# Kernel optimization log

Measured on AMD Instinct MI355X. Metric: run time of the kernel, lower is better.

Reference implementation:

```python
import jax, jax.numpy as jnp
import numpy as np

NEG_INF = -1e9  # large negative for masking (avoid NaN rows under -inf with fully masked rows)
LEAKY_SLOPE = 0.2

def setup_inputs() -> dict:
    key = jax.random.key(0)
    k1, k2, k3, k4, k5 = jax.random.split(key, 5)
    N, in_dim, out_dim = 8192, 512, 64
    x = jax.random.normal(k1, (N, in_dim), dtype=jnp.float32)
    adj = jax.random.randint(k2, (N, N), 0, 2, dtype=jnp.int32)
    W = jax.random.normal(k3, (out_dim, in_dim), dtype=jnp.float32) * (1.0 / np.sqrt(in_dim))
    a_src = jax.random.normal(k4, (out_dim,), dtype=jnp.float32)
    a_dst = jax.random.normal(k5, (out_dim,), dtype=jnp.float32)
    return {"x": x, "adj": adj, "W": W, "a_src": a_src, "a_dst": a_dst}

def reference(x, adj, W, a_src, a_dst):
    # Linear projection: Wh[n, d]
    Wh = x @ W.T
    # Additive GAT attention: e[i, j] = LeakyReLU(a_src . Wh_i + a_dst . Wh_j)
    s = Wh @ a_src  # [N]
    d = Wh @ a_dst  # [N]
    e = jax.nn.leaky_relu(s[:, None] + d[None, :], negative_slope=LEAKY_SLOPE)  # [N, N]
    e = jnp.where(adj > 0, e, NEG_INF)
    alpha = jax.nn.softmax(e, axis=1)  # [N, N]
    # Dropout on alpha is identity in eval/reference mode.
    h_prime = alpha @ Wh  # [N, out_dim]
    return h_prime
```

## Files before the change

kernel.cpp:

```cpp
#include <hip/hip_runtime.h>

#define GN 8192
#define IN_DIM 512
#define ODIM 64
#define SLOPE 0.2f

typedef __attribute__((ext_vector_type(4))) float  f32x4;
typedef __attribute__((ext_vector_type(4))) int    i32x4;
typedef __attribute__((ext_vector_type(8))) short  bf16x8;
typedef __attribute__((ext_vector_type(4))) unsigned short u16x4;

static __device__ __forceinline__ float bf2f(unsigned short u) {
    return __uint_as_float(((unsigned)u) << 16);
}
static __device__ __forceinline__ unsigned short f2bf(float f) {
    union { float f; unsigned u; } c; c.f = f;
    unsigned b = c.u;
    return (unsigned short)((b + 0x7fffu + ((b >> 16) & 1u)) >> 16);
}

extern "C" __global__ void gat_detect(const unsigned* __restrict__ xw,
                                      int* __restrict__ flag)
{
    if (threadIdx.x == 0) {
        int votes = 0;
        for (int t = 0; t < 64; ++t) {
            unsigned e = (xw[t] >> 23) & 0xffu;
            votes += (e > 60u && e < 180u) ? 1 : 0;
        }
        *flag = (votes >= 32) ? 1 : 0;
    }
}

static __device__ __forceinline__ bf16x8 load8(const void* p, size_t off, int f32) {
    if (f32) {
        f32x4 lo = *(const f32x4*)((const float*)p + off);
        f32x4 hi = *(const f32x4*)((const float*)p + off + 4);
        bf16x8 r;
        #pragma unroll
        for (int q = 0; q < 4; ++q) {
            r[q]     = (short)f2bf(lo[q]);
            r[4 + q] = (short)f2bf(hi[q]);
        }
        return r;
    }
    return *(const bf16x8*)((const ushort*)p + off);
}

extern "C" __global__ __launch_bounds__(256)
void gat_proj(const void* __restrict__ x_, const void* __restrict__ W_,
              const void* __restrict__ as_, const void* __restrict__ ad_,
              const int* __restrict__ flag,
              ushort* __restrict__ WhT, float* __restrict__ s_arr,
              float* __restrict__ d_arr, int* __restrict__ dmax_bits)
{
    const int wave = threadIdx.x >> 6;
    const int lane = threadIdx.x & 63;
    const int quad = lane >> 4;
    const int lq   = lane & 15;
    const int i0   = blockIdx.x * 64 + wave * 16;
    const int f32  = *flag;

    f32x4 acc[4] = {{0,0,0,0},{0,0,0,0},{0,0,0,0},{0,0,0,0}};
    const size_t arow = (size_t)(i0 + lq) * IN_DIM;
    #pragma unroll 2
    for (int k0 = 0; k0 < IN_DIM; k0 += 32) {
        const int kk = k0 + quad * 8;
        bf16x8 a  = load8(x_, arow + kk, f32);
        bf16x8 b0 = load8(W_, (size_t)( 0 + lq) * IN_DIM + kk, f32);
        bf16x8 b1 = load8(W_, (size_t)(16 + lq) * IN_DIM + kk, f32);
        bf16x8 b2 = load8(W_, (size_t)(32 + lq) * IN_DIM + kk, f32);
        bf16x8 b3 = load8(W_, (size_t)(48 + lq) * IN_DIM + kk, f32);
        acc[0] = __builtin_amdgcn_mfma_f32_16x16x32_bf16(a, b0, acc[0], 0, 0, 0);
        acc[1] = __builtin_amdgcn_mfma_f32_16x16x32_bf16(a, b1, acc[1], 0, 0, 0);
        acc[2] = __builtin_amdgcn_mfma_f32_16x16x32_bf16(a, b2, acc[2], 0, 0, 0);
        acc[3] = __builtin_amdgcn_mfma_f32_16x16x32_bf16(a, b3, acc[3], 0, 0, 0);
    }
    float av_s[4], av_d[4];
    #pragma unroll
    for (int t = 0; t < 4; ++t) {
        const int n = t * 16 + lq;
        av_s[t] = f32 ? ((const float*)as_)[n] : bf2f(((const ushort*)as_)[n]);
        av_d[t] = f32 ? ((const float*)ad_)[n] : bf2f(((const ushort*)ad_)[n]);
    }
    #pragma unroll
    for (int t = 0; t < 4; ++t) {
        u16x4 pk;
        #pragma unroll
        for (int r = 0; r < 4; ++r) pk[r] = f2bf(acc[t][r]);
        *(u16x4*)(WhT + (size_t)(t * 16 + lq) * GN + i0 + quad * 4) = pk;
    }
    float ps[4], pd[4];
    #pragma unroll
    for (int r = 0; r < 4; ++r) {
        float s = 0.f, d = 0.f;
        #pragma unroll
        for (int t = 0; t < 4; ++t) {
            s = fmaf(acc[t][r], av_s[t], s);
            d = fmaf(acc[t][r], av_d[t], d);
        }
        #pragma unroll
        for (int off = 1; off < 16; off <<= 1) {
            s += __shfl_xor(s, off);
            d += __shfl_xor(d, off);
        }
        ps[r] = s; pd[r] = d;
    }
    if (lq == 0) {
        float dmx = -1e30f;
        #pragma unroll
        for (int r = 0; r < 4; ++r) {
            s_arr[i0 + quad * 4 + r] = ps[r];
            d_arr[i0 + quad * 4 + r] = pd[r];
            dmx = fmaxf(dmx, pd[r]);
        }
        if (dmx > 0.f) atomicMax(dmax_bits, __float_as_int(dmx));
    }
}

extern "C" __global__ __launch_bounds__(256, 4)
void gat_attn(const int* __restrict__ adj, const ushort* __restrict__ WhT,
              const float* __restrict__ s_arr, const float* __restrict__ d_arr,
              const int* __restrict__ dmax_bits,
              float* __restrict__ accum, float* __restrict__ lsum)
{
    const int JCH = GN / 8;
    const int ib   = blockIdx.x & 127;
    const int js   = blockIdx.x >> 7;
    const int wave = threadIdx.x >> 6;
    const int lane = threadIdx.x & 63;
    const int quad = lane >> 4;
    const int lq   = lane & 15;
    const int i = ib * 64 + wave * 16 + lq;
    const float dmax = __int_as_float(*dmax_bits);
    const float si = s_arr[i];
    const float tb = si + dmax;
    const float mi = fmaxf(tb, SLOPE * tb);
    const int jbase = js * JCH;
    f32x4 acc0 = {0,0,0,0}, acc1 = {0,0,0,0}, acc2 = {0,0,0,0}, acc3 = {0,0,0,0};
    float lacc = 0.f;
    const int* adjrow = adj + (size_t)i * GN;
    const int iters = JCH / 32;

    int j0 = jbase + quad * 8;
    i32x4 av0 = *(const i32x4*)(adjrow + j0);
    i32x4 av1 = *(const i32x4*)(adjrow + j0 + 4);
    f32x4 dv0 = *(const f32x4*)(d_arr + j0);
    f32x4 dv1 = *(const f32x4*)(d_arr + j0 + 4);

    for (int it = 0; it < iters; ++it) {
        const int jc = j0;
        const int jn = (it + 1 < iters) ? (j0 + 32) : (jbase + quad * 8);
        i32x4 nav0 = *(const i32x4*)(adjrow + jn);
        i32x4 nav1 = *(const i32x4*)(adjrow + jn + 4);
        f32x4 ndv0 = *(const f32x4*)(d_arr + jn);
        f32x4 ndv1 = *(const f32x4*)(d_arr + jn + 4);
        bf16x8 b0 = *(const bf16x8*)(WhT + (size_t)( 0 + lq) * GN + jc);
        bf16x8 b1 = *(const bf16x8*)(WhT + (size_t)(16 + lq) * GN + jc);
        bf16x8 b2 = *(const bf16x8*)(WhT + (size_t)(32 + lq) * GN + jc);
        bf16x8 b3 = *(const bf16x8*)(WhT + (size_t)(48 + lq) * GN + jc);

        float w[8];
        #pragma unroll
        for (int q = 0; q < 4; ++q) {
            float e0 = si + dv0[q];
            e0 = fmaxf(e0, SLOPE * e0);
            float v0 = __expf(e0 - mi);
            w[q] = (av0[q] > 0) ? v0 : 0.f;
            float e1 = si + dv1[q];
            e1 = fmaxf(e1, SLOPE * e1);
            float v1 = __expf(e1 - mi);
            w[4 + q] = (av1[q] > 0) ? v1 : 0.f;
        }
        bf16x8 af;
        #pragma unroll
        for (int q = 0; q < 8; ++q) {
            unsigned short wb = f2bf(w[q]);
            af[q] = (short)wb;
            lacc += bf2f(wb);
        }
        acc0 = __builtin_amdgcn_mfma_f32_16x16x32_bf16(af, b0, acc0, 0, 0, 0);
        acc1 = __builtin_amdgcn_mfma_f32_16x16x32_bf16(af, b1, acc1, 0, 0, 0);
        acc2 = __builtin_amdgcn_mfma_f32_16x16x32_bf16(af, b2, acc2, 0, 0, 0);
        acc3 = __builtin_amdgcn_mfma_f32_16x16x32_bf16(af, b3, acc3, 0, 0, 0);

        av0 = nav0; av1 = nav1; dv0 = ndv0; dv1 = ndv1;
        j0 += 32;
    }
    lacc += __shfl_xor(lacc, 16);
    lacc += __shfl_xor(lacc, 32);
    if (quad == 0) atomicAdd(&lsum[i], lacc);
    const int orow = ib * 64 + wave * 16 + quad * 4;
    #pragma unroll
    for (int r = 0; r < 4; ++r) {
        atomicAdd(&accum[(size_t)(orow + r) * ODIM +  0 + lq], acc0[r]);
        atomicAdd(&accum[(size_t)(orow + r) * ODIM + 16 + lq], acc1[r]);
        atomicAdd(&accum[(size_t)(orow + r) * ODIM + 32 + lq], acc2[r]);
        atomicAdd(&accum[(size_t)(orow + r) * ODIM + 48 + lq], acc3[r]);
    }
}

extern "C" __global__ __launch_bounds__(256)
void gat_final(const float* __restrict__ accum, const float* __restrict__ lsum,
               const int* __restrict__ flag, void* __restrict__ out)
{
    const int idx = blockIdx.x * 256 + threadIdx.x;
    const float v = accum[idx] / lsum[idx >> 6];
    if (*flag) ((float*)out)[idx] = v;
    else       ((ushort*)out)[idx] = f2bf(v);
}

extern "C" void kernel_launch(void* const* d_in, const int* in_sizes, int n_in,
                              void* d_out, int out_size, void* d_ws, size_t ws_size,
                              hipStream_t stream)
{
    const void* x     = d_in[0];
    const int*  adj   = (const int*)d_in[1];
    const void* W     = d_in[2];
    const void* a_src = d_in[3];
    const void* a_dst = d_in[4];

    char* ws = (char*)d_ws;
    size_t off = 0;
    float* accum = (float*)(ws + off);  off += (size_t)GN * ODIM * 4;
    float* lsum  = (float*)(ws + off);  off += (size_t)GN * 4;
    int* dmax_bits = (int*)(ws + off);  off += 128;
    size_t zero_bytes = off;
    int* dflag = (int*)(ws + off);      off += 128;
    float* s_arr = (float*)(ws + off);  off += (size_t)GN * 4;
    float* d_arr = (float*)(ws + off);  off += (size_t)GN * 4;
    ushort* WhT  = (ushort*)(ws + off); off += (size_t)ODIM * GN * 2;

    hipMemsetAsync(ws, 0, zero_bytes, stream);
    gat_detect<<<1, 64, 0, stream>>>((const unsigned*)x, dflag);
    gat_proj<<<GN / 64, 256, 0, stream>>>(x, W, a_src, a_dst, dflag, WhT, s_arr, d_arr, dmax_bits);
    gat_attn<<<1024, 256, 0, stream>>>(adj, WhT, s_arr, d_arr, dmax_bits, accum, lsum);
    gat_final<<<GN * ODIM / 256, 256, 0, stream>>>(accum, lsum, dflag, d_out);
}
```

Before: 488.3 us.

## Pre-pack adjacency into bitmask alongside projection and consume bits in attention

A new prep kernel streams the int32 adjacency matrix once and packs it into a 1-bit-per-edge mask with wave ballots. It runs in the same launch as the projection blocks, which now also do the fp32/bf16 format detection themselves, so a separate detect kernel is no longer needed. The attention kernel reads 32-bit mask words instead of full int rows, which cuts its memory traffic and load instructions, and it doubles the j-split to 16 for more parallelism. The cost is an extra 8MB bitmask write and read and twice as many atomic adds into the accumulator.

```diff
diff --git a/kernel.cpp b/kernel.cpp
--- a/kernel.cpp
+++ b/kernel.cpp
@@ -4,6 +4,10 @@
 #define IN_DIM 512
 #define ODIM 64
 #define SLOPE 0.2f
+#define PB 128
+#define CB 2048
+#define JSPLIT 16
+#define JCH (GN / JSPLIT)
 
 typedef __attribute__((ext_vector_type(4))) float  f32x4;
 typedef __attribute__((ext_vector_type(4))) int    i32x4;
@@ -17,19 +21,6 @@
     union { float f; unsigned u; } c; c.f = f;
     unsigned b = c.u;
     return (unsigned short)((b + 0x7fffu + ((b >> 16) & 1u)) >> 16);
-}
-
-extern "C" __global__ void gat_detect(const unsigned* __restrict__ xw,
-                                      int* __restrict__ flag)
-{
-    if (threadIdx.x == 0) {
-        int votes = 0;
-        for (int t = 0; t < 64; ++t) {
-            unsigned e = (xw[t] >> 23) & 0xffu;
-            votes += (e > 60u && e < 180u) ? 1 : 0;
-        }
-        *flag = (votes >= 32) ? 1 : 0;
-    }
 }
 
 static __device__ __forceinline__ bf16x8 load8(const void* p, size_t off, int f32) {
@@ -48,18 +39,48 @@
 }
 
 extern "C" __global__ __launch_bounds__(256)
-void gat_proj(const void* __restrict__ x_, const void* __restrict__ W_,
+void gat_prep(const void* __restrict__ x_, const void* __restrict__ W_,
               const void* __restrict__ as_, const void* __restrict__ ad_,
-              const int* __restrict__ flag,
+              const int* __restrict__ adj, unsigned long long* __restrict__ bits64,
               ushort* __restrict__ WhT, float* __restrict__ s_arr,
-              float* __restrict__ d_arr, int* __restrict__ dmax_bits)
+              float* __restrict__ d_arr, int* __restrict__ dmax_bits,
+              int* __restrict__ dflag)
 {
     const int wave = threadIdx.x >> 6;
     const int lane = threadIdx.x & 63;
+
+    if (blockIdx.x >= PB) {
+        const int wid = (blockIdx.x - PB) * 4 + wave;
+        const size_t stride = (size_t)CB * 4 * 256;
+        #pragma unroll 2
+        for (int it = 0; it < 32; ++it) {
+            const size_t base = (size_t)wid * 256 + (size_t)it * stride;
+            int a0 = adj[base +   0 + lane];
+            int a1 = adj[base +  64 + lane];
+            int a2 = adj[base + 128 + lane];
+            int a3 = adj[base + 192 + lane];
+            unsigned long long b0 = __ballot(a0 > 0);
+            unsigned long long b1 = __ballot(a1 > 0);
+            unsigned long long b2 = __ballot(a2 > 0);
+            unsigned long long b3 = __ballot(a3 > 0);
+            if (lane == 0) {
+                ulonglong2* p = (ulonglong2*)(bits64 + base / 64);
+                p[0] = make_ulonglong2(b0, b1);
+                p[1] = make_ulonglong2(b2, b3);
+            }
+        }
+        return;
+    }
+
+    unsigned xw = ((const unsigned*)x_)[lane];
+    unsigned ef = (xw >> 23) & 0xffu;
+    unsigned long long vt = __ballot(ef > 60u && ef < 180u);
+    const int f32 = (__popcll(vt) >= 32) ? 1 : 0;
+    if (blockIdx.x == 0 && threadIdx.x == 0) *dflag = f32;
+
     const int quad = lane >> 4;
     const int lq   = lane & 15;
     const int i0   = blockIdx.x * 64 + wave * 16;
-    const int f32  = *flag;
 
     f32x4 acc[4] = {{0,0,0,0},{0,0,0,0},{0,0,0,0},{0,0,0,0}};
     const size_t arow = (size_t)(i0 + lq) * IN_DIM;
@@ -119,12 +140,11 @@
 }
 
 extern "C" __global__ __launch_bounds__(256, 4)
-void gat_attn(const int* __restrict__ adj, const ushort* __restrict__ WhT,
+void gat_attn(const unsigned* __restrict__ bits32, const ushort* __restrict__ WhT,
               const float* __restrict__ s_arr, const float* __restrict__ d_arr,
               const int* __restrict__ dmax_bits,
               float* __restrict__ accum, float* __restrict__ lsum)
 {
-    const int JCH = GN / 8;
     const int ib   = blockIdx.x & 127;
     const int js   = blockIdx.x >> 7;
     const int wave = threadIdx.x >> 6;
@@ -139,53 +159,46 @@
     const int jbase = js * JCH;
     f32x4 acc0 = {0,0,0,0}, acc1 = {0,0,0,0}, acc2 = {0,0,0,0}, acc3 = {0,0,0,0};
     float lacc = 0.f;
-    const int* adjrow = adj + (size_t)i * GN;
-    const int iters = JCH / 32;
-
-    int j0 = jbase + quad * 8;
-    i32x4 av0 = *(const i32x4*)(adjrow + j0);
-    i32x4 av1 = *(const i32x4*)(adjrow + j0 + 4);
-    f32x4 dv0 = *(const f32x4*)(d_arr + j0);
-    f32x4 dv1 = *(const f32x4*)(d_arr + j0 + 4);
-
-    for (int it = 0; it < iters; ++it) {
-        const int jc = j0;
-        const int jn = (it + 1 < iters) ? (j0 + 32) : (jbase + quad * 8);
-        i32x4 nav0 = *(const i32x4*)(adjrow + jn);
-        i32x4 nav1 = *(const i32x4*)(adjrow + jn + 4);
-        f32x4 ndv0 = *(const f32x4*)(d_arr + jn);
-        f32x4 ndv1 = *(const f32x4*)(d_arr + jn + 4);
-        bf16x8 b0 = *(const bf16x8*)(WhT + (size_t)( 0 + lq) * GN + jc);
-        bf16x8 b1 = *(const bf16x8*)(WhT + (size_t)(16 + lq) * GN + jc);
-        bf16x8 b2 = *(const bf16x8*)(WhT + (size_t)(32 + lq) * GN + jc);
-        bf16x8 b3 = *(const bf16x8*)(WhT + (size_t)(48 + lq) * GN + jc);
-
-        float w[8];
-        #pragma unroll
-        for (int q = 0; q < 4; ++q) {
-            float e0 = si + dv0[q];
-            e0 = fmaxf(e0, SLOPE * e0);
-            float v0 = __expf(e0 - mi);
-            w[q] = (av0[q] > 0) ? v0 : 0.f;
-            float e1 = si + dv1[q];
-            e1 = fmaxf(e1, SLOPE * e1);
-            float v1 = __expf(e1 - mi);
-            w[4 + q] = (av1[q] > 0) ? v1 : 0.f;
-        }
-        bf16x8 af;
-        #pragma unroll
-        for (int q = 0; q < 8; ++q) {
-            unsigned short wb = f2bf(w[q]);
-            af[q] = (short)wb;
-            lacc += bf2f(wb);
-        }
-        acc0 = __builtin_amdgcn_mfma_f32_16x16x32_bf16(af, b0, acc0, 0, 0, 0);
-        acc1 = __builtin_amdgcn_mfma_f32_16x16x32_bf16(af, b1, acc1, 0, 0, 0);
-        acc2 = __builtin_amdgcn_mfma_f32_16x16x32_bf16(af, b2, acc2, 0, 0, 0);
-        acc3 = __builtin_amdgcn_mfma_f32_16x16x32_bf16(af, b3, acc3, 0, 0, 0);
-
-        av0 = nav0; av1 = nav1; dv0 = ndv0; dv1 = ndv1;
-        j0 += 32;
+    const unsigned* bitrow = bits32 + (size_t)i * (GN / 32) + js * (JCH / 32);
+
+    #pragma unroll 1
+    for (int it4 = 0; it4 < JCH / 128; ++it4) {
+        i32x4 bw = *(const i32x4*)(bitrow + it4 * 4);
+        #pragma unroll
+        for (int sub = 0; sub < 4; ++sub) {
+            const int it = it4 * 4 + sub;
+            const int j0 = jbase + it * 32 + quad * 8;
+            const unsigned m8 = (((unsigned)bw[sub]) >> (quad * 8)) & 0xffu;
+            f32x4 dv0 = *(const f32x4*)(d_arr + j0);
+            f32x4 dv1 = *(const f32x4*)(d_arr + j0 + 4);
+            bf16x8 b0 = *(const bf16x8*)(WhT + (size_t)( 0 + lq) * GN + j0);
+            bf16x8 b1 = *(const bf16x8*)(WhT + (size_t)(16 + lq) * GN + j0);
+            bf16x8 b2 = *(const bf16x8*)(WhT + (size_t)(32 + lq) * GN + j0);
+            bf16x8 b3 = *(const bf16x8*)(WhT + (size_t)(48 + lq) * GN + j0);
+            float w[8];
+            #pragma unroll
+            for (int q = 0; q < 4; ++q) {
+                float e0 = si + dv0[q];
+                e0 = fmaxf(e0, SLOPE * e0);
+                float v0 = __expf(e0 - mi);
+                w[q] = ((m8 >> q) & 1u) ? v0 : 0.f;
+                float e1 = si + dv1[q];
+                e1 = fmaxf(e1, SLOPE * e1);
+                float v1 = __expf(e1 - mi);
+                w[4 + q] = ((m8 >> (4 + q)) & 1u) ? v1 : 0.f;
+            }
+            bf16x8 af;
+            #pragma unroll
+            for (int q = 0; q < 8; ++q) {
+                unsigned short wb = f2bf(w[q]);
+                af[q] = (short)wb;
+                lacc += bf2f(wb);
+            }
+            acc0 = __builtin_amdgcn_mfma_f32_16x16x32_bf16(af, b0, acc0, 0, 0, 0);
+            acc1 = __builtin_amdgcn_mfma_f32_16x16x32_bf16(af, b1, acc1, 0, 0, 0);
+            acc2 = __builtin_amdgcn_mfma_f32_16x16x32_bf16(af, b2, acc2, 0, 0, 0);
+            acc3 = __builtin_amdgcn_mfma_f32_16x16x32_bf16(af, b3, acc3, 0, 0, 0);
+        }
     }
     lacc += __shfl_xor(lacc, 16);
     lacc += __shfl_xor(lacc, 32);
@@ -230,10 +243,13 @@
     float* s_arr = (float*)(ws + off);  off += (size_t)GN * 4;
     float* d_arr = (float*)(ws + off);  off += (size_t)GN * 4;
     ushort* WhT  = (ushort*)(ws + off); off += (size_t)ODIM * GN * 2;
+    unsigned long long* bits = (unsigned long long*)(ws + off);
+    off += (size_t)GN * GN / 8;
 
     hipMemsetAsync(ws, 0, zero_bytes, stream);
-    gat_detect<<<1, 64, 0, stream>>>((const unsigned*)x, dflag);
-    gat_proj<<<GN / 64, 256, 0, stream>>>(x, W, a_src, a_dst, dflag, WhT, s_arr, d_arr, dmax_bits);
-    gat_attn<<<1024, 256, 0, stream>>>(adj, WhT, s_arr, d_arr, dmax_bits, accum, lsum);
+    gat_prep<<<PB + CB, 256, 0, stream>>>(x, W, a_src, a_dst, adj, bits,
+                                          WhT, s_arr, d_arr, dmax_bits, dflag);
+    gat_attn<<<128 * JSPLIT, 256, 0, stream>>>((const unsigned*)bits, WhT,
+                                               s_arr, d_arr, dmax_bits, accum, lsum);
     gat_final<<<GN * ODIM / 256, 256, 0, stream>>>(accum, lsum, dflag, d_out);
 }
```

Result: faster. 457.5 us (-6.3%).
